# Performance work log

Measured on AMD Instinct MI355X. Metric: run time of the kernel, lower is better.

The kernel has to match this reference:

```python
import jax, jax.numpy as jnp
import numpy as np

B, S, D = 1024, 192, 512
MAX_ITEMS, NUM_LAYERS = 64, 3
LN_EPS = 1e-5


def setup_inputs() -> dict:
    key = jax.random.key(0)
    k_tok, k_pad, k_item, k_layer, k_temp = jax.random.split(key, 5)
    token_embeddings = jax.random.normal(k_tok, (B, S, D), dtype=jnp.float32)
    # Left-padded mask: zeros then contiguous ones until the end of the row.
    pad_len = jax.random.randint(k_pad, (B,), 0, S)  # at least 1 real token
    attention_mask = (jnp.arange(S)[None, :] >= pad_len[:, None]).astype(jnp.int32)
    item_pos_emb = 0.01 * jax.random.normal(k_item, (MAX_ITEMS, D), dtype=jnp.float32)
    layer_emb = 0.01 * jax.random.normal(k_layer, (NUM_LAYERS, D), dtype=jnp.float32)
    temporal_decay = 0.02 * jax.random.normal(k_temp, (MAX_ITEMS, D), dtype=jnp.float32)
    ln_weight = jnp.ones((D,), dtype=jnp.float32)
    ln_bias = jnp.zeros((D,), dtype=jnp.float32)
    return {
        "token_embeddings": token_embeddings,
        "attention_mask": attention_mask,
        "item_pos_emb": item_pos_emb,
        "layer_emb": layer_emb,
        "temporal_decay": temporal_decay,
        "ln_weight": ln_weight,
        "ln_bias": ln_bias,
    }


def reference(token_embeddings, attention_mask, item_pos_emb, layer_emb,
              temporal_decay, ln_weight, ln_bias):
    mask = attention_mask > 0                              # (B, S) bool
    has_content = jnp.any(mask, axis=1)                    # (B,)
    start = jnp.argmax(mask, axis=1)                       # first non-pad index
    end = S - jnp.argmax(mask[:, ::-1], axis=1)            # last non-pad index + 1
    idx = jnp.arange(S)[None, :]                           # (1, S)
    pos = idx - start[:, None]                             # content-relative position
    in_range = (pos >= 0) & (idx < end[:, None]) & has_content[:, None]
    pos_c = jnp.clip(pos, 0)
    item_idx = jnp.where(in_range, pos_c // NUM_LAYERS, 0)  # (B, S)
    layer_idx = jnp.where(in_range, pos_c % NUM_LAYERS, 0)
    add = item_pos_emb[item_idx] + layer_emb[layer_idx] + temporal_decay[item_idx]
    enhanced = token_embeddings + jnp.where(in_range[..., None], add, 0.0)
    # LayerNorm over last dim
    mu = jnp.mean(enhanced, axis=-1, keepdims=True)
    var = jnp.mean(jnp.square(enhanced - mu), axis=-1, keepdims=True)
    normed = (enhanced - mu) * jax.lax.rsqrt(var + LN_EPS) * ln_weight + ln_bias
    # zero out padding (dropout is identity in eval mode)
    return normed * attention_mask[..., None].astype(normed.dtype)
```

## Files before the change

### kernel.cpp

```cpp
#include <hip/hip_runtime.h>

#define BB 1024
#define SS 192
#define DD 512
#define NUM_LAYERS 3
#define LN_EPS 1e-5f

__global__ __launch_bounds__(256) void start_kernel(const int* __restrict__ mask,
                                                    int* __restrict__ start) {
    const int b = (blockIdx.x * blockDim.x + threadIdx.x) >> 6;
    const int lane = threadIdx.x & 63;
    if (b >= BB) return;
    const int* m = mask + b * SS;
    const unsigned long long b0 = __ballot(m[lane] > 0);
    const unsigned long long b1 = __ballot(m[lane + 64] > 0);
    const unsigned long long b2 = __ballot(m[lane + 128] > 0);
    int idx;
    if (b0)      idx = __ffsll(b0) - 1;
    else if (b1) idx = 64 + __ffsll(b1) - 1;
    else if (b2) idx = 128 + __ffsll(b2) - 1;
    else         idx = 0;
    if (lane == 0) start[b] = idx;
}

__global__ __launch_bounds__(256) void fused_kernel(
    const float* __restrict__ tok,
    const int* __restrict__ mask,
    const float* __restrict__ item_pos,
    const float* __restrict__ layer_emb,
    const float* __restrict__ decay,
    const float* __restrict__ lnw,
    const float* __restrict__ lnb,
    const int* __restrict__ start,
    float* __restrict__ out)
{
    const int wid = threadIdx.x >> 6;
    const int lane = threadIdx.x & 63;
    const int row = blockIdx.x * 4 + wid;
    const int b = row / SS;
    const int s = row - b * SS;

    float4* o4 = reinterpret_cast<float4*>(out + (size_t)row * DD);

    if (mask[row] == 0) {
        const float4 z = make_float4(0.f, 0.f, 0.f, 0.f);
        o4[lane] = z;
        o4[lane + 64] = z;
        return;
    }

    const int st = start[b];
    const int pos = s - st;
    const int item_idx = pos / NUM_LAYERS;
    const int layer_idx = pos - item_idx * NUM_LAYERS;

    const float4* x4 = reinterpret_cast<const float4*>(tok + (size_t)row * DD);
    float4 xv0 = x4[lane];
    float4 xv1 = x4[lane + 64];

    const float4* i4 = reinterpret_cast<const float4*>(item_pos + item_idx * DD);
    const float4* l4 = reinterpret_cast<const float4*>(layer_emb + layer_idx * DD);
    const float4* d4 = reinterpret_cast<const float4*>(decay + item_idx * DD);

    const float4 i0 = i4[lane], i1 = i4[lane + 64];
    const float4 l0 = l4[lane], l1 = l4[lane + 64];
    const float4 dd0 = d4[lane], dd1 = d4[lane + 64];

    xv0.x += i0.x + l0.x + dd0.x;  xv0.y += i0.y + l0.y + dd0.y;
    xv0.z += i0.z + l0.z + dd0.z;  xv0.w += i0.w + l0.w + dd0.w;
    xv1.x += i1.x + l1.x + dd1.x;  xv1.y += i1.y + l1.y + dd1.y;
    xv1.z += i1.z + l1.z + dd1.z;  xv1.w += i1.w + l1.w + dd1.w;

    float sum = xv0.x + xv0.y + xv0.z + xv0.w + xv1.x + xv1.y + xv1.z + xv1.w;
    float sq  = xv0.x * xv0.x + xv0.y * xv0.y + xv0.z * xv0.z + xv0.w * xv0.w
              + xv1.x * xv1.x + xv1.y * xv1.y + xv1.z * xv1.z + xv1.w * xv1.w;

    #pragma unroll
    for (int m = 32; m > 0; m >>= 1) {
        sum += __shfl_xor(sum, m, 64);
        sq  += __shfl_xor(sq,  m, 64);
    }

    const float mu  = sum * (1.0f / DD);
    const float var = sq * (1.0f / DD) - mu * mu;
    const float inv = rsqrtf(var + LN_EPS);

    const float4* w4 = reinterpret_cast<const float4*>(lnw);
    const float4* bb4 = reinterpret_cast<const float4*>(lnb);
    const float4 w0 = w4[lane], w1 = w4[lane + 64];
    const float4 b0 = bb4[lane], b1 = bb4[lane + 64];

    float4 ov0, ov1;
    ov0.x = (xv0.x - mu) * inv * w0.x + b0.x;
    ov0.y = (xv0.y - mu) * inv * w0.y + b0.y;
    ov0.z = (xv0.z - mu) * inv * w0.z + b0.z;
    ov0.w = (xv0.w - mu) * inv * w0.w + b0.w;
    ov1.x = (xv1.x - mu) * inv * w1.x + b1.x;
    ov1.y = (xv1.y - mu) * inv * w1.y + b1.y;
    ov1.z = (xv1.z - mu) * inv * w1.z + b1.z;
    ov1.w = (xv1.w - mu) * inv * w1.w + b1.w;

    o4[lane] = ov0;
    o4[lane + 64] = ov1;
}

extern "C" void kernel_launch(void* const* d_in, const int* in_sizes, int n_in,
                              void* d_out, int out_size, void* d_ws, size_t ws_size,
                              hipStream_t stream) {
    const float* tok       = (const float*)d_in[0];
    const int*   mask      = (const int*)d_in[1];
    const float* item_pos  = (const float*)d_in[2];
    const float* layer_emb = (const float*)d_in[3];
    const float* decay     = (const float*)d_in[4];
    const float* lnw       = (const float*)d_in[5];
    const float* lnb       = (const float*)d_in[6];
    float* out = (float*)d_out;

    int* start = (int*)d_ws;

    start_kernel<<<(BB * 64 + 255) / 256, 256, 0, stream>>>(mask, start);
    fused_kernel<<<(BB * SS) / 4, 256, 0, stream>>>(tok, mask, item_pos, layer_emb,
                                                    decay, lnw, lnb, start, out);
}
```

Baseline: 157.9 us.

## Precompute positional add table and use persistent grid-stride LayerNorm waves

A prep kernel now builds a combined per-position add table (item + layer + decay embeddings) alongside the per-batch start index, so each row does one table gather instead of three. The fused kernel becomes a persistent grid-stride loop with 2048 blocks, hoisting the LayerNorm weight and bias loads out of the per-row work. It also drops the per-row mask read by comparing the position against the start index. This trades a small extra workspace table and less parallel slack for fewer loads per row on a bandwidth-bound kernel.

```diff
diff --git a/kernel.cpp b/kernel.cpp
--- a/kernel.cpp
+++ b/kernel.cpp
@@ -5,30 +5,55 @@
 #define DD 512
 #define NUM_LAYERS 3
 #define LN_EPS 1e-5f
+#define NROWS (BB * SS)
+#define FUSED_BLOCKS 2048
+#define NWAVES (FUSED_BLOCKS * 4)
 
-__global__ __launch_bounds__(256) void start_kernel(const int* __restrict__ mask,
-                                                    int* __restrict__ start) {
-    const int b = (blockIdx.x * blockDim.x + threadIdx.x) >> 6;
-    const int lane = threadIdx.x & 63;
-    if (b >= BB) return;
-    const int* m = mask + b * SS;
-    const unsigned long long b0 = __ballot(m[lane] > 0);
-    const unsigned long long b1 = __ballot(m[lane + 64] > 0);
-    const unsigned long long b2 = __ballot(m[lane + 128] > 0);
-    int idx;
-    if (b0)      idx = __ffsll(b0) - 1;
-    else if (b1) idx = 64 + __ffsll(b1) - 1;
-    else if (b2) idx = 128 + __ffsll(b2) - 1;
-    else         idx = 0;
-    if (lane == 0) start[b] = idx;
+__global__ __launch_bounds__(256) void prep_kernel(
+    const int* __restrict__ mask,
+    const float* __restrict__ item_pos,
+    const float* __restrict__ layer_emb,
+    const float* __restrict__ decay,
+    float* __restrict__ add_tab,
+    int* __restrict__ start)
+{
+    if (blockIdx.x < SS) {
+        const int p = blockIdx.x;
+        const int t = threadIdx.x;
+        if (t < DD / 4) {
+            const int item = p / NUM_LAYERS;
+            const int layer = p - item * NUM_LAYERS;
+            const float4 iv = reinterpret_cast<const float4*>(item_pos + item * DD)[t];
+            const float4 lv = reinterpret_cast<const float4*>(layer_emb + layer * DD)[t];
+            const float4 dv = reinterpret_cast<const float4*>(decay + item * DD)[t];
+            float4 v;
+            v.x = iv.x + lv.x + dv.x;
+            v.y = iv.y + lv.y + dv.y;
+            v.z = iv.z + lv.z + dv.z;
+            v.w = iv.w + lv.w + dv.w;
+            reinterpret_cast<float4*>(add_tab + p * DD)[t] = v;
+        }
+    } else {
+        const int b = (blockIdx.x - SS) * 4 + (threadIdx.x >> 6);
+        const int lane = threadIdx.x & 63;
+        if (b < BB) {
+            const int* m = mask + b * SS;
+            const unsigned long long b0 = __ballot(m[lane] > 0);
+            const unsigned long long b1 = __ballot(m[lane + 64] > 0);
+            const unsigned long long b2 = __ballot(m[lane + 128] > 0);
+            int idx;
+            if (b0)      idx = __ffsll(b0) - 1;
+            else if (b1) idx = 64 + __ffsll(b1) - 1;
+            else if (b2) idx = 128 + __ffsll(b2) - 1;
+            else         idx = SS;
+            if (lane == 0) start[b] = idx;
+        }
+    }
 }
 
 __global__ __launch_bounds__(256) void fused_kernel(
     const float* __restrict__ tok,
-    const int* __restrict__ mask,
-    const float* __restrict__ item_pos,
-    const float* __restrict__ layer_emb,
-    const float* __restrict__ decay,
+    const float* __restrict__ add_tab,
     const float* __restrict__ lnw,
     const float* __restrict__ lnb,
     const int* __restrict__ start,
@@ -36,72 +61,70 @@
 {
     const int wid = threadIdx.x >> 6;
     const int lane = threadIdx.x & 63;
-    const int row = blockIdx.x * 4 + wid;
-    const int b = row / SS;
-    const int s = row - b * SS;
+    const int l0 = lane;
+    const int l1 = lane + 64;
 
-    float4* o4 = reinterpret_cast<float4*>(out + (size_t)row * DD);
+    const float4 w0 = reinterpret_cast<const float4*>(lnw)[l0];
+    const float4 w1 = reinterpret_cast<const float4*>(lnw)[l1];
+    const float4 c0 = reinterpret_cast<const float4*>(lnb)[l0];
+    const float4 c1 = reinterpret_cast<const float4*>(lnb)[l1];
 
-    if (mask[row] == 0) {
-        const float4 z = make_float4(0.f, 0.f, 0.f, 0.f);
-        o4[lane] = z;
-        o4[lane + 64] = z;
-        return;
+    const int wave = blockIdx.x * 4 + wid;
+
+    for (int row = wave; row < NROWS; row += NWAVES) {
+        const int b = row / SS;
+        const int s = row - b * SS;
+        const int st = start[b];
+
+        float4* o4 = reinterpret_cast<float4*>(out + (size_t)row * DD);
+
+        if (s < st) {
+            const float4 z = make_float4(0.f, 0.f, 0.f, 0.f);
+            o4[l0] = z;
+            o4[l1] = z;
+            continue;
+        }
+
+        const int pos = s - st;
+
+        const float4* x4 = reinterpret_cast<const float4*>(tok + (size_t)row * DD);
+        float4 xv0 = x4[l0];
+        float4 xv1 = x4[l1];
+
+        const float4* a4 = reinterpret_cast<const float4*>(add_tab + pos * DD);
+        const float4 a0 = a4[l0];
+        const float4 a1 = a4[l1];
+
+        xv0.x += a0.x;  xv0.y += a0.y;  xv0.z += a0.z;  xv0.w += a0.w;
+        xv1.x += a1.x;  xv1.y += a1.y;  xv1.z += a1.z;  xv1.w += a1.w;
+
+        float sum = xv0.x + xv0.y + xv0.z + xv0.w + xv1.x + xv1.y + xv1.z + xv1.w;
+        float sq  = xv0.x * xv0.x + xv0.y * xv0.y + xv0.z * xv0.z + xv0.w * xv0.w
+                  + xv1.x * xv1.x + xv1.y * xv1.y + xv1.z * xv1.z + xv1.w * xv1.w;
+
+        #pragma unroll
+        for (int m = 32; m > 0; m >>= 1) {
+            sum += __shfl_xor(sum, m, 64);
+            sq  += __shfl_xor(sq,  m, 64);
+        }
+
+        const float mu  = sum * (1.0f / DD);
+        const float var = sq * (1.0f / DD) - mu * mu;
+        const float inv = rsqrtf(var + LN_EPS);
+
+        float4 ov0, ov1;
+        ov0.x = (xv0.x - mu) * inv * w0.x + c0.x;
+        ov0.y = (xv0.y - mu) * inv * w0.y + c0.y;
+        ov0.z = (xv0.z - mu) * inv * w0.z + c0.z;
+        ov0.w = (xv0.w - mu) * inv * w0.w + c0.w;
+        ov1.x = (xv1.x - mu) * inv * w1.x + c1.x;
+        ov1.y = (xv1.y - mu) * inv * w1.y + c1.y;
+        ov1.z = (xv1.z - mu) * inv * w1.z + c1.z;
+        ov1.w = (xv1.w - mu) * inv * w1.w + c1.w;
+
+        o4[l0] = ov0;
+        o4[l1] = ov1;
     }
-
-    const int st = start[b];
-    const int pos = s - st;
-    const int item_idx = pos / NUM_LAYERS;
-    const int layer_idx = pos - item_idx * NUM_LAYERS;
-
-    const float4* x4 = reinterpret_cast<const float4*>(tok + (size_t)row * DD);
-    float4 xv0 = x4[lane];
-    float4 xv1 = x4[lane + 64];
-
-    const float4* i4 = reinterpret_cast<const float4*>(item_pos + item_idx * DD);
-    const float4* l4 = reinterpret_cast<const float4*>(layer_emb + layer_idx * DD);
-    const float4* d4 = reinterpret_cast<const float4*>(decay + item_idx * DD);
-
-    const float4 i0 = i4[lane], i1 = i4[lane + 64];
-    const float4 l0 = l4[lane], l1 = l4[lane + 64];
-    const float4 dd0 = d4[lane], dd1 = d4[lane + 64];
-
-    xv0.x += i0.x + l0.x + dd0.x;  xv0.y += i0.y + l0.y + dd0.y;
-    xv0.z += i0.z + l0.z + dd0.z;  xv0.w += i0.w + l0.w + dd0.w;
-    xv1.x += i1.x + l1.x + dd1.x;  xv1.y += i1.y + l1.y + dd1.y;
-    xv1.z += i1.z + l1.z + dd1.z;  xv1.w += i1.w + l1.w + dd1.w;
-
-    float sum = xv0.x + xv0.y + xv0.z + xv0.w + xv1.x + xv1.y + xv1.z + xv1.w;
-    float sq  = xv0.x * xv0.x + xv0.y * xv0.y + xv0.z * xv0.z + xv0.w * xv0.w
-              + xv1.x * xv1.x + xv1.y * xv1.y + xv1.z * xv1.z + xv1.w * xv1.w;
-
-    #pragma unroll
-    for (int m = 32; m > 0; m >>= 1) {
-        sum += __shfl_xor(sum, m, 64);
-        sq  += __shfl_xor(sq,  m, 64);
-    }
-
-    const float mu  = sum * (1.0f / DD);
-    const float var = sq * (1.0f / DD) - mu * mu;
-    const float inv = rsqrtf(var + LN_EPS);
-
-    const float4* w4 = reinterpret_cast<const float4*>(lnw);
-    const float4* bb4 = reinterpret_cast<const float4*>(lnb);
-    const float4 w0 = w4[lane], w1 = w4[lane + 64];
-    const float4 b0 = bb4[lane], b1 = bb4[lane + 64];
-
-    float4 ov0, ov1;
-    ov0.x = (xv0.x - mu) * inv * w0.x + b0.x;
-    ov0.y = (xv0.y - mu) * inv * w0.y + b0.y;
-    ov0.z = (xv0.z - mu) * inv * w0.z + b0.z;
-    ov0.w = (xv0.w - mu) * inv * w0.w + b0.w;
-    ov1.x = (xv1.x - mu) * inv * w1.x + b1.x;
-    ov1.y = (xv1.y - mu) * inv * w1.y + b1.y;
-    ov1.z = (xv1.z - mu) * inv * w1.z + b1.z;
-    ov1.w = (xv1.w - mu) * inv * w1.w + b1.w;
-
-    o4[lane] = ov0;
-    o4[lane + 64] = ov1;
 }
 
 extern "C" void kernel_launch(void* const* d_in, const int* in_sizes, int n_in,
@@ -116,9 +139,10 @@
     const float* lnb       = (const float*)d_in[6];
     float* out = (float*)d_out;
 
-    int* start = (int*)d_ws;
+    float* add_tab = (float*)d_ws;
+    int* start = (int*)((char*)d_ws + (size_t)SS * DD * sizeof(float));
 
-    start_kernel<<<(BB * 64 + 255) / 256, 256, 0, stream>>>(mask, start);
-    fused_kernel<<<(BB * SS) / 4, 256, 0, stream>>>(tok, mask, item_pos, layer_emb,
-                                                    decay, lnw, lnb, start, out);
+    prep_kernel<<<SS + 256, 256, 0, stream>>>(mask, item_pos, layer_emb, decay,
+                                              add_tab, start);
+    fused_kernel<<<FUSED_BLOCKS, 256, 0, stream>>>(tok, add_tab, lnw, lnb, start, out);
 }
```

After: 147.1 us. -6.8%, faster.
